# Kernel optimization log

Measured on AMD Instinct MI355X. Metric: run time of the kernel, lower is better.

Reference implementation:

```python
import jax, jax.numpy as jnp
import numpy as np

P_DROP = 0.31881923790897965  # torch.dropout p from the original module


def setup_inputs() -> dict:
    key = jax.random.key(0)
    k1, k2, k3, k4 = jax.random.split(key, 4)
    B, H, S, KV, D = 1, 16, 2048, 4096, 64  # KV = 2*S so the [S,2S] triu|tril mask lines up
    query = jax.random.normal(k1, (B, H, S, D), dtype=jnp.float32)
    key_t = jax.random.normal(k2, (B, H, KV, D), dtype=jnp.float32)
    value = jax.random.normal(k3, (B, H, KV, D), dtype=jnp.float32)
    # deterministic dropout keep-mask, keep prob = 1 - p
    drop_mask = jax.random.bernoulli(k4, 1.0 - P_DROP, (B, H, S, KV))
    return {"query": query, "key": key_t, "value": value, "drop_mask": drop_mask}


def _structured_mask(S, dtype):
    # torch.cat([triu(ones(S,S,bool),1), tril(ones(S,S,bool))], dim=-1) -> [S, 2S]
    # bool mask is ADDED to scores (promotes to 0/1 floats), exactly as in the original.
    triu = jnp.triu(jnp.ones((S, S), dtype=bool), 1)
    tril = jnp.tril(jnp.ones((S, S), dtype=bool))
    return jnp.concatenate([triu, tril], axis=-1).astype(dtype)  # [S, 2S]


def reference(query, key, value, drop_mask):
    B, H, S, D = query.shape
    scale = jnp.asarray(1.0 / np.sqrt(D), query.dtype)
    mask = _structured_mask(S, query.dtype)  # [S, 2S] of 0/1
    # qk: [B,H,S,KV]
    qk = jnp.einsum('bhsd,bhkd->bhsk', query, key) * scale + mask
    attn = jax.nn.softmax(qk, axis=-1)
    keep_scale = jnp.asarray(1.0 / (1.0 - P_DROP), attn.dtype)
    attn = jnp.where(drop_mask, attn * keep_scale, jnp.zeros((), attn.dtype))
    return jnp.einsum('bhsk,bhkd->bhsd', attn, value)
```

## Files before the change

kernel.cpp:

```cpp
#include <hip/hip_runtime.h>
#include <hip/hip_bf16.h>


#define H_   16
#define S_   2048
#define KV_  4096
#define D_   64
#define NSPLIT 2
#define CPB  32

using bf16x8 = __attribute__((ext_vector_type(8))) __bf16;
using bf16x4 = __attribute__((ext_vector_type(4))) __bf16;
using f32x4  = __attribute__((ext_vector_type(4))) float;
using uintx4 = __attribute__((ext_vector_type(4))) unsigned;

constexpr float KEEP_SCALE = (float)(1.0 / (1.0 - 0.31881923790897965));
#define C_SC  0.18033688011112043f
#define C_ONE -10.098865286222744f
#define C_ZRO -11.541560327111707f

#define WS_FLAG 0
#define WS_K    256
#define WS_V    (WS_K + 8388608)
#define WS_PART (WS_V + 8388608)
#define WS_LS   (WS_PART + 16777216)

__device__ __forceinline__ void gld16(const void* g, void* l) {
    __builtin_amdgcn_global_load_lds(
        (const __attribute__((address_space(1))) unsigned*)g,
        (__attribute__((address_space(3))) unsigned*)l, 16, 0, 0);
}

__global__ void detect_mask(const unsigned* __restrict__ m, int* __restrict__ flag) {
    __shared__ int bad;
    if (threadIdx.x == 0) bad = 0;
    __syncthreads();
    int ok = 1;
    for (int i = threadIdx.x; i < 4096; i += blockDim.x) {
        unsigned w = m[i];
        if (w > 1u && w != 0x3F800000u) ok = 0;
    }
    if (!ok) atomicOr(&bad, 1);
    __syncthreads();
    if (threadIdx.x == 0) *flag = bad;
}

__global__ __launch_bounds__(256)
void conv_k(const float* __restrict__ K, char* __restrict__ out) {
    const unsigned u = blockIdx.x * 256 + threadIdx.x;
    const unsigned w = u & 511;
    const unsigned row = w >> 3;
    const unsigned dcol = (((w & 7) * 16) ^ ((row & 7) << 4)) >> 1;
    const unsigned tile = u >> 9, h = tile >> 6, c = tile & 63;
    const float* src = K + (((size_t)h * KV_) + c * 64 + row) * D_ + dcol;
    f32x4 f0 = *(const f32x4*)src;
    f32x4 f1 = *(const f32x4*)(src + 4);
    bf16x8 b;
    #pragma unroll
    for (int e = 0; e < 4; ++e) { b[e] = (__bf16)f0[e]; b[4 + e] = (__bf16)f1[e]; }
    *(bf16x8*)(out + (size_t)u * 16) = b;
}

__global__ __launch_bounds__(256)
void conv_v(const float* __restrict__ V, char* __restrict__ out) {
    __shared__ __bf16 T[64][72];
    const int tile = blockIdx.x;
    const int h = tile >> 6, c = tile & 63;
    const float* src = V + ((size_t)h * KV_ + c * 64) * D_;
    const int tid = threadIdx.x;
    #pragma unroll
    for (int r = 0; r < 4; ++r) {
        const int off = r * 1024 + tid * 4;
        const int kv = off >> 6, d = off & 63;
        f32x4 f = *(const f32x4*)(src + off);
        #pragma unroll
        for (int e = 0; e < 4; ++e) T[d + e][kv] = (__bf16)f[e];
    }
    __syncthreads();
    char* dst = out + (size_t)tile * 8192;
    #pragma unroll
    for (int r = 0; r < 2; ++r) {
        const int u = r * 256 + tid;
        const int d = u >> 3;
        const int kv0 = ((((u & 7) * 16) ^ ((d & 7) << 4))) >> 1;
        *(bf16x8*)(dst + (size_t)u * 16) = *(const bf16x8*)&T[d][kv0];
    }
}

__global__ __launch_bounds__(512, 4)
void attn_fwd(const float* __restrict__ Q,
              const unsigned char* __restrict__ Mb,
              const int* __restrict__ flagp,
              const char* __restrict__ Ktiles,
              const char* __restrict__ Vtiles,
              float* __restrict__ Part,
              float* __restrict__ Ls)
{
    __shared__ char smem[49152];

    const int tid  = threadIdx.x;
    const int wave = tid >> 6, lane = tid & 63;
    const int lq   = lane & 15, g = lane >> 4;
    const int swz  = (lq & 7) << 4;

    const int b  = blockIdx.x;
    const int wg = (b & 7) * 64 + (b >> 3);
    const int h  = wg >> 5;
    const int qt = (wg >> 1) & 15, split = wg & 1;
    const int q0w = qt * 128 + wave * 16;
    const int q_g = q0w + lq;

    const bool byteMode = (*flagp != 0);
    const unsigned* Mw = (const unsigned*)Mb;

    bf16x8 bq[2];
    {
        const float* qrow = Q + ((size_t)h * S_ + q_g) * D_ + g * 8;
        #pragma unroll
        for (int kk = 0; kk < 2; ++kk) {
            f32x4 f0 = *(const f32x4*)(qrow + 32 * kk);
            f32x4 f1 = *(const f32x4*)(qrow + 32 * kk + 4);
            bf16x8 bb;
            #pragma unroll
            for (int e = 0; e < 4; ++e) { bb[e] = (__bf16)f0[e]; bb[4 + e] = (__bf16)f1[e]; }
            bq[kk] = bb;
        }
    }

    const char* gK = Ktiles + (size_t)h * 64 * 8192;
    const char* gV = Vtiles + (size_t)h * 64 * 8192;
    char* Pb = smem + 32768 + wave * 2048;

    float lsum = 0.f;
    f32x4 acc[4] = {};

    auto stage = [&](int buf, int c) {
        const char* sk = gK + (size_t)c * 8192 + tid * 16;
        const char* sv = gV + (size_t)c * 8192 + tid * 16;
        char* dk = smem + buf * 16384 + tid * 16;
        gld16(sk, dk);
        gld16(sv, dk + 8192);
    };

    unsigned mreg[16];
    auto load_bits = [&](int cc) {
        if (byteMode) {
            const unsigned char* base = Mb + ((size_t)h * S_ + q0w) * KV_ + (size_t)cc * 64 + lane;
            #pragma unroll
            for (int i = 0; i < 16; ++i) mreg[i] = base[(size_t)i * KV_];
        } else {
            const unsigned* base = Mw + ((size_t)h * S_ + q0w) * KV_ + (size_t)cc * 64 + lane;
            #pragma unroll
            for (int i = 0; i < 16; ++i) mreg[i] = base[(size_t)i * KV_];
        }
    };
    auto ballot_bits = [&]() -> unsigned long long {
        unsigned long long sav = 0;
        #pragma unroll
        for (int i = 0; i < 16; ++i) {
            unsigned long long bal = __ballot(mreg[i] != 0u);
            if (lq == i) sav = bal;
        }
        return sav;
    };

    const int cs = split * CPB, ce = cs + CPB;
    load_bits(cs);
    stage(0, cs);
    unsigned long long mb_cur = ballot_bits();
    __syncthreads();
    int cur = 0;

    for (int c = cs; c < ce; ++c) {
        const bool more = (c + 1 < ce);
        if (more) load_bits(c + 1);
        if (more) stage(cur ^ 1, c + 1);
        const unsigned long long mb = mb_cur;
        const char* Kb = smem + cur * 16384;
        const char* Vb = Kb + 8192;

        f32x4 st[4] = {};
        __builtin_amdgcn_s_setprio(1);
        #pragma unroll
        for (int t = 0; t < 4; ++t) {
            #pragma unroll
            for (int kk = 0; kk < 2; ++kk) {
                bf16x8 ak = *(const bf16x8*)(Kb + (16 * t + lq) * 128 + ((16 * g + 64 * kk) ^ swz));
                st[t] = __builtin_amdgcn_mfma_f32_16x16x32_bf16(ak, bq[kk], st[t], 0, 0, 0);
            }
        }
        __builtin_amdgcn_s_setprio(0);

        #pragma unroll
        for (int t = 0; t < 4; ++t) {
            bf16x4 pb;
            #pragma unroll
            for (int i = 0; i < 4; ++i) {
                const int kvl = 16 * t + 4 * g + i;
                const int kvg = c * 64 + kvl;
                const bool one = (kvg < S_) ? (kvg > q_g) : (kvg - S_ <= q_g);
                float v = fmaf(st[t][i], C_SC, one ? C_ONE : C_ZRO);
                float pp = exp2f(v);
                lsum += pp;
                pb[i] = (__bf16)(((mb >> kvl) & 1) ? pp : 0.f);
            }
            *(bf16x4*)(Pb + lq * 128 + ((32 * t + 8 * g) ^ swz)) = pb;
        }

        asm volatile("s_waitcnt lgkmcnt(0)" ::: "memory");
        __builtin_amdgcn_sched_barrier(0);

        __builtin_amdgcn_s_setprio(1);
        #pragma unroll
        for (int c2 = 0; c2 < 2; ++c2) {
            bf16x8 ap = *(const bf16x8*)(Pb + lq * 128 + ((64 * c2 + 16 * g) ^ swz));
            #pragma unroll
            for (int nt = 0; nt < 4; ++nt) {
                bf16x8 bv = *(const bf16x8*)(Vb + (16 * nt + lq) * 128 + ((64 * c2 + 16 * g) ^ swz));
                acc[nt] = __builtin_amdgcn_mfma_f32_16x16x32_bf16(ap, bv, acc[nt], 0, 0, 0);
            }
        }
        __builtin_amdgcn_s_setprio(0);

        if (more) mb_cur = ballot_bits();

        __syncthreads();
        cur ^= 1;
    }

    lsum += __shfl_xor(lsum, 16);
    lsum += __shfl_xor(lsum, 32);
    if (g == 0) Ls[((size_t)split * H_ + h) * S_ + q_g] = lsum;

    float* pa = Part + (((size_t)split * H_ + h) * S_ + q0w + 4 * g) * D_;
    #pragma unroll
    for (int i = 0; i < 4; ++i)
        #pragma unroll
        for (int nt = 0; nt < 4; ++nt)
            pa[i * D_ + nt * 16 + lq] = acc[nt][i];
}

__global__ __launch_bounds__(256)
void combine(const float* __restrict__ Part, const float* __restrict__ Ls,
             float* __restrict__ Out) {
    const int idx = blockIdx.x * 256 + threadIdx.x;
    const int r  = idx >> 4;
    const int dg = (idx & 15) * 4;
    const f32x4 a = *(const f32x4*)(Part + (size_t)r * D_ + dg);
    const f32x4 b = *(const f32x4*)(Part + (size_t)(H_ * S_ + r) * D_ + dg);
    const float l = Ls[r] + Ls[H_ * S_ + r];
    const float s = KEEP_SCALE / l;
    f32x4 o;
    #pragma unroll
    for (int e = 0; e < 4; ++e) o[e] = (a[e] + b[e]) * s;
    *(f32x4*)(Out + (size_t)r * D_ + dg) = o;
}

extern "C" void kernel_launch(void* const* d_in, const int* in_sizes, int n_in,
                              void* d_out, int out_size, void* d_ws, size_t ws_size,
                              hipStream_t stream) {
    const float* Q = (const float*)d_in[0];
    const float* K = (const float*)d_in[1];
    const float* V = (const float*)d_in[2];
    const unsigned char* M = (const unsigned char*)d_in[3];
    char* ws = (char*)d_ws;
    int* flag = (int*)(ws + WS_FLAG);
    char* kt = ws + WS_K;
    char* vt = ws + WS_V;
    float* part = (float*)(ws + WS_PART);
    float* ls = (float*)(ws + WS_LS);

    detect_mask<<<1, 256, 0, stream>>>((const unsigned*)M, flag);
    conv_k<<<2048, 256, 0, stream>>>(K, kt);
    conv_v<<<1024, 256, 0, stream>>>(V, vt);
    attn_fwd<<<512, 512, 0, stream>>>(Q, M, flag, kt, vt, part, ls);
    combine<<<2048, 256, 0, stream>>>(part, ls, (float*)d_out);
}
```

Baseline: 175.3 us.

## Halve workgroup size and batch dropout-mask loads four chunks at a time

The attention kernel now runs 1024 workgroups of 256 threads, each covering 64 query rows instead of 128, with the K/V staging done as four 16-byte copies per thread and LDS cut to 40 KB. The dropout mask is fetched as wide vector non-temporal loads covering four 64-column chunks at once, then ballot-packed into four bitmasks, replacing a narrow per-chunk load-and-ballot each iteration. The aim is more coalesced, higher-throughput reads of the large mask stream and better occupancy and scheduling from smaller blocks. In exchange it holds more registers for the mask data and launches twice as many blocks that each restage the same K/V tiles.

```diff
diff --git a/kernel.cpp b/kernel.cpp
--- a/kernel.cpp
+++ b/kernel.cpp
@@ -87,8 +87,7 @@
     }
 }
 
-__global__ __launch_bounds__(512, 4)
-void attn_fwd(const float* __restrict__ Q,
+__global__ void attn_fwd(const float* __restrict__ Q,
               const unsigned char* __restrict__ Mb,
               const int* __restrict__ flagp,
               const char* __restrict__ Ktiles,
@@ -96,7 +95,7 @@
               float* __restrict__ Part,
               float* __restrict__ Ls)
 {
-    __shared__ char smem[49152];
+    __shared__ char smem[40960];
 
     const int tid  = threadIdx.x;
     const int wave = tid >> 6, lane = tid & 63;
@@ -104,10 +103,10 @@
     const int swz  = (lq & 7) << 4;
 
     const int b  = blockIdx.x;
-    const int wg = (b & 7) * 64 + (b >> 3);
-    const int h  = wg >> 5;
-    const int qt = (wg >> 1) & 15, split = wg & 1;
-    const int q0w = qt * 128 + wave * 16;
+    const int wg = (b & 7) * 128 + (b >> 3);
+    const int h  = wg >> 6;
+    const int qt = (wg >> 1) & 31, split = wg & 1;
+    const int q0w = qt * 64 + wave * 16;
     const int q_g = q0w + lq;
 
     const bool byteMode = (*flagp != 0);
@@ -138,94 +137,108 @@
         const char* sk = gK + (size_t)c * 8192 + tid * 16;
         const char* sv = gV + (size_t)c * 8192 + tid * 16;
         char* dk = smem + buf * 16384 + tid * 16;
-        gld16(sk, dk);
-        gld16(sv, dk + 8192);
+        gld16(sk,        dk);
+        gld16(sk + 4096, dk + 4096);
+        gld16(sv,        dk + 8192);
+        gld16(sv + 4096, dk + 12288);
     };
 
-    unsigned mreg[16];
-    auto load_bits = [&](int cc) {
+    uintx4  mr[16];
+    unsigned mrb[16];
+    auto load_quad = [&](int c0) {
         if (byteMode) {
-            const unsigned char* base = Mb + ((size_t)h * S_ + q0w) * KV_ + (size_t)cc * 64 + lane;
-            #pragma unroll
-            for (int i = 0; i < 16; ++i) mreg[i] = base[(size_t)i * KV_];
+            const unsigned char* bp = Mb + ((size_t)h * S_ + q0w) * KV_ + (size_t)c0 * 64 + 4 * lane;
+            #pragma unroll
+            for (int r = 0; r < 16; ++r)
+                mrb[r] = __builtin_nontemporal_load((const unsigned*)(bp + (size_t)r * KV_));
         } else {
-            const unsigned* base = Mw + ((size_t)h * S_ + q0w) * KV_ + (size_t)cc * 64 + lane;
-            #pragma unroll
-            for (int i = 0; i < 16; ++i) mreg[i] = base[(size_t)i * KV_];
+            const unsigned* wp = Mw + ((size_t)h * S_ + q0w) * KV_ + (size_t)c0 * 64 + 4 * lane;
+            #pragma unroll
+            for (int r = 0; r < 16; ++r)
+                mr[r] = __builtin_nontemporal_load((const uintx4*)(wp + (size_t)r * KV_));
         }
     };
-    auto ballot_bits = [&]() -> unsigned long long {
-        unsigned long long sav = 0;
-        #pragma unroll
-        for (int i = 0; i < 16; ++i) {
-            unsigned long long bal = __ballot(mreg[i] != 0u);
-            if (lq == i) sav = bal;
-        }
-        return sav;
+    unsigned long long balv[4];
+    auto ballot_quad = [&]() {
+        #pragma unroll
+        for (int r = 0; r < 16; ++r) {
+            #pragma unroll
+            for (int j = 0; j < 4; ++j) {
+                const bool pred = byteMode ? (((mrb[r] >> (8 * j)) & 0xFFu) != 0u)
+                                           : (mr[r][j] != 0u);
+                unsigned long long bal = __ballot(pred);
+                if (lq == r) balv[j] = bal;
+            }
+        }
     };
 
     const int cs = split * CPB, ce = cs + CPB;
-    load_bits(cs);
+    load_quad(cs);
     stage(0, cs);
-    unsigned long long mb_cur = ballot_bits();
+    ballot_quad();
     __syncthreads();
     int cur = 0;
 
-    for (int c = cs; c < ce; ++c) {
-        const bool more = (c + 1 < ce);
-        if (more) load_bits(c + 1);
-        if (more) stage(cur ^ 1, c + 1);
-        const unsigned long long mb = mb_cur;
-        const char* Kb = smem + cur * 16384;
-        const char* Vb = Kb + 8192;
-
-        f32x4 st[4] = {};
-        __builtin_amdgcn_s_setprio(1);
-        #pragma unroll
-        for (int t = 0; t < 4; ++t) {
-            #pragma unroll
-            for (int kk = 0; kk < 2; ++kk) {
-                bf16x8 ak = *(const bf16x8*)(Kb + (16 * t + lq) * 128 + ((16 * g + 64 * kk) ^ swz));
-                st[t] = __builtin_amdgcn_mfma_f32_16x16x32_bf16(ak, bq[kk], st[t], 0, 0, 0);
-            }
-        }
-        __builtin_amdgcn_s_setprio(0);
-
-        #pragma unroll
-        for (int t = 0; t < 4; ++t) {
-            bf16x4 pb;
-            #pragma unroll
-            for (int i = 0; i < 4; ++i) {
-                const int kvl = 16 * t + 4 * g + i;
-                const int kvg = c * 64 + kvl;
-                const bool one = (kvg < S_) ? (kvg > q_g) : (kvg - S_ <= q_g);
-                float v = fmaf(st[t][i], C_SC, one ? C_ONE : C_ZRO);
-                float pp = exp2f(v);
-                lsum += pp;
-                pb[i] = (__bf16)(((mb >> kvl) & 1) ? pp : 0.f);
-            }
-            *(bf16x4*)(Pb + lq * 128 + ((32 * t + 8 * g) ^ swz)) = pb;
-        }
-
-        asm volatile("s_waitcnt lgkmcnt(0)" ::: "memory");
-        __builtin_amdgcn_sched_barrier(0);
-
-        __builtin_amdgcn_s_setprio(1);
-        #pragma unroll
-        for (int c2 = 0; c2 < 2; ++c2) {
-            bf16x8 ap = *(const bf16x8*)(Pb + lq * 128 + ((64 * c2 + 16 * g) ^ swz));
-            #pragma unroll
-            for (int nt = 0; nt < 4; ++nt) {
-                bf16x8 bv = *(const bf16x8*)(Vb + (16 * nt + lq) * 128 + ((64 * c2 + 16 * g) ^ swz));
-                acc[nt] = __builtin_amdgcn_mfma_f32_16x16x32_bf16(ap, bv, acc[nt], 0, 0, 0);
-            }
-        }
-        __builtin_amdgcn_s_setprio(0);
-
-        if (more) mb_cur = ballot_bits();
-
-        __syncthreads();
-        cur ^= 1;
+    for (int qd = 0; qd < CPB / 4; ++qd) {
+        const bool moreq = (qd + 1 < CPB / 4);
+        if (moreq) load_quad(cs + 4 * (qd + 1));
+
+        #pragma unroll
+        for (int g4 = 0; g4 < 4; ++g4) {
+            const int c = cs + 4 * qd + g4;
+            if (c + 1 < ce) stage(cur ^ 1, c + 1);
+            const char* Kb = smem + cur * 16384;
+            const char* Vb = Kb + 8192;
+
+            f32x4 st[4] = {};
+            __builtin_amdgcn_s_setprio(1);
+            #pragma unroll
+            for (int t = 0; t < 4; ++t) {
+                #pragma unroll
+                for (int kk = 0; kk < 2; ++kk) {
+                    bf16x8 ak = *(const bf16x8*)(Kb + (16 * t + lq) * 128 + ((16 * g + 64 * kk) ^ swz));
+                    st[t] = __builtin_amdgcn_mfma_f32_16x16x32_bf16(ak, bq[kk], st[t], 0, 0, 0);
+                }
+            }
+            __builtin_amdgcn_s_setprio(0);
+
+            const int shb = 16 * g4 + g;
+            #pragma unroll
+            for (int t = 0; t < 4; ++t) {
+                bf16x4 pb;
+                #pragma unroll
+                for (int i = 0; i < 4; ++i) {
+                    const int kvl = 16 * t + 4 * g + i;
+                    const int kvg = c * 64 + kvl;
+                    const bool one = (kvg < S_) ? (kvg > q_g) : (kvg - S_ <= q_g);
+                    float v = fmaf(st[t][i], C_SC, one ? C_ONE : C_ZRO);
+                    float pp = exp2f(v);
+                    lsum += pp;
+                    pb[i] = (__bf16)(((balv[i] >> (shb + 4 * t)) & 1) ? pp : 0.f);
+                }
+                *(bf16x4*)(Pb + lq * 128 + ((32 * t + 8 * g) ^ swz)) = pb;
+            }
+
+            asm volatile("s_waitcnt lgkmcnt(0)" ::: "memory");
+            __builtin_amdgcn_sched_barrier(0);
+
+            __builtin_amdgcn_s_setprio(1);
+            #pragma unroll
+            for (int c2 = 0; c2 < 2; ++c2) {
+                bf16x8 ap = *(const bf16x8*)(Pb + lq * 128 + ((64 * c2 + 16 * g) ^ swz));
+                #pragma unroll
+                for (int nt = 0; nt < 4; ++nt) {
+                    bf16x8 bv = *(const bf16x8*)(Vb + (16 * nt + lq) * 128 + ((64 * c2 + 16 * g) ^ swz));
+                    acc[nt] = __builtin_amdgcn_mfma_f32_16x16x32_bf16(ap, bv, acc[nt], 0, 0, 0);
+                }
+            }
+            __builtin_amdgcn_s_setprio(0);
+
+            __syncthreads();
+            cur ^= 1;
+        }
+
+        if (moreq) ballot_quad();
     }
 
     lsum += __shfl_xor(lsum, 16);
@@ -273,6 +286,6 @@
     detect_mask<<<1, 256, 0, stream>>>((const unsigned*)M, flag);
     conv_k<<<2048, 256, 0, stream>>>(K, kt);
     conv_v<<<1024, 256, 0, stream>>>(V, vt);
-    attn_fwd<<<512, 512, 0, stream>>>(Q, M, flag, kt, vt, part, ls);
+    attn_fwd<<<1024, 256, 0, stream>>>(Q, M, flag, kt, vt, part, ls);
     combine<<<2048, 256, 0, stream>>>(part, ls, (float*)d_out);
 }
```

Result: slower. 453.3 us (+158.5%).

## Triple-buffer K/V tiles and prefetch mask two chunks ahead with manual vmcnt waits

Applied to the files above, without the earlier changes.

Moves the K/V LDS staging from double to triple buffering and issues tile loads two chunks ahead. Dropout mask bits are likewise prefetched two chunks ahead, and __syncthreads is replaced with explicit s_waitcnt vmcnt counts plus s_barrier, so global loads stay in flight across iterations. The aim is to hide global-memory latency for the mask and tile loads. In exchange LDS grows from 48KB to 64KB, which may cut occupancy at 4 blocks per CU. The hand-counted vmcnt values are fragile: a wrong count can race or stall.

```diff
diff --git a/kernel.cpp b/kernel.cpp
--- a/kernel.cpp
+++ b/kernel.cpp
@@ -12,7 +12,6 @@
 using bf16x8 = __attribute__((ext_vector_type(8))) __bf16;
 using bf16x4 = __attribute__((ext_vector_type(4))) __bf16;
 using f32x4  = __attribute__((ext_vector_type(4))) float;
-using uintx4 = __attribute__((ext_vector_type(4))) unsigned;
 
 constexpr float KEEP_SCALE = (float)(1.0 / (1.0 - 0.31881923790897965));
 #define C_SC  0.18033688011112043f
@@ -96,7 +95,7 @@
               float* __restrict__ Part,
               float* __restrict__ Ls)
 {
-    __shared__ char smem[49152];
+    __shared__ char smem[65536];
 
     const int tid  = threadIdx.x;
     const int wave = tid >> 6, lane = tid & 63;
@@ -129,12 +128,13 @@
 
     const char* gK = Ktiles + (size_t)h * 64 * 8192;
     const char* gV = Vtiles + (size_t)h * 64 * 8192;
-    char* Pb = smem + 32768 + wave * 2048;
+    char* Pb = smem + 49152 + wave * 2048;
 
     float lsum = 0.f;
     f32x4 acc[4] = {};
 
-    auto stage = [&](int buf, int c) {
+    auto stage = [&](int c) {
+        const int buf = c % 3;
         const char* sk = gK + (size_t)c * 8192 + tid * 16;
         const char* sv = gV + (size_t)c * 8192 + tid * 16;
         char* dk = smem + buf * 16384 + tid * 16;
@@ -154,30 +154,36 @@
             for (int i = 0; i < 16; ++i) mreg[i] = base[(size_t)i * KV_];
         }
     };
-    auto ballot_bits = [&]() -> unsigned long long {
+    unsigned long long balv;
+    auto ballot_bits = [&]() {
         unsigned long long sav = 0;
         #pragma unroll
         for (int i = 0; i < 16; ++i) {
             unsigned long long bal = __ballot(mreg[i] != 0u);
             if (lq == i) sav = bal;
         }
-        return sav;
+        balv = sav;
     };
 
     const int cs = split * CPB, ce = cs + CPB;
+
     load_bits(cs);
-    stage(0, cs);
-    unsigned long long mb_cur = ballot_bits();
-    __syncthreads();
-    int cur = 0;
+    stage(cs);
+    stage(cs + 1);
+    asm volatile("s_waitcnt vmcnt(4)" ::: "memory");
+    __builtin_amdgcn_sched_barrier(0);
+    ballot_bits();
+    load_bits(cs + 1);
+    asm volatile("s_waitcnt vmcnt(18)" ::: "memory");
+    __builtin_amdgcn_sched_barrier(0);
+    __builtin_amdgcn_s_barrier();
 
     for (int c = cs; c < ce; ++c) {
-        const bool more = (c + 1 < ce);
-        if (more) load_bits(c + 1);
-        if (more) stage(cur ^ 1, c + 1);
-        const unsigned long long mb = mb_cur;
-        const char* Kb = smem + cur * 16384;
+        const bool m1 = (c + 1 < ce), m2 = (c + 2 < ce);
+        if (m2) stage(c + 2);
+        const char* Kb = smem + (c % 3) * 16384;
         const char* Vb = Kb + 8192;
+        const unsigned long long mb = balv;
 
         f32x4 st[4] = {};
         __builtin_amdgcn_s_setprio(1);
@@ -222,10 +228,20 @@
         }
         __builtin_amdgcn_s_setprio(0);
 
-        if (more) mb_cur = ballot_bits();
-
-        __syncthreads();
-        cur ^= 1;
+        if (m1) {
+            if (m2) { asm volatile("s_waitcnt vmcnt(2)" ::: "memory"); }
+            else    { asm volatile("s_waitcnt vmcnt(0)" ::: "memory"); }
+            __builtin_amdgcn_sched_barrier(0);
+            ballot_bits();
+            if (m2) load_bits(c + 2);
+        }
+
+        if (m1) {
+            if (m2) { asm volatile("s_waitcnt vmcnt(18)" ::: "memory"); }
+            else    { asm volatile("s_waitcnt vmcnt(0)" ::: "memory"); }
+            __builtin_amdgcn_sched_barrier(0);
+            __builtin_amdgcn_s_barrier();
+        }
     }
 
     lsum += __shfl_xor(lsum, 16);
```

Result: no change. 174.1 us (-0.7%).

## Double-buffer dropout mask registers and replace syncthreads with explicit vmcnt waits

Applied to the files above, without the earlier changes.

Unrolls the KV-chunk loop by two, using two register banks for the dropout-mask loads so the mask for chunk c+2 is in flight while chunk c is computed. Full __syncthreads is replaced by hand-placed s_waitcnt vmcnt counts plus s_barrier, so only the needed outstanding loads are waited on. The aim is to keep more global loads in flight and avoid the full-drain wait that syncthreads implies. The cost is more register use and fragile hard-coded vmcnt counts that must match the exact number of issued loads.

```diff
diff --git a/kernel.cpp b/kernel.cpp
--- a/kernel.cpp
+++ b/kernel.cpp
@@ -12,7 +12,6 @@
 using bf16x8 = __attribute__((ext_vector_type(8))) __bf16;
 using bf16x4 = __attribute__((ext_vector_type(4))) __bf16;
 using f32x4  = __attribute__((ext_vector_type(4))) float;
-using uintx4 = __attribute__((ext_vector_type(4))) unsigned;
 
 constexpr float KEEP_SCALE = (float)(1.0 / (1.0 - 0.31881923790897965));
 #define C_SC  0.18033688011112043f
@@ -142,41 +141,35 @@
         gld16(sv, dk + 8192);
     };
 
-    unsigned mreg[16];
-    auto load_bits = [&](int cc) {
-        if (byteMode) {
-            const unsigned char* base = Mb + ((size_t)h * S_ + q0w) * KV_ + (size_t)cc * 64 + lane;
-            #pragma unroll
-            for (int i = 0; i < 16; ++i) mreg[i] = base[(size_t)i * KV_];
-        } else {
-            const unsigned* base = Mw + ((size_t)h * S_ + q0w) * KV_ + (size_t)cc * 64 + lane;
-            #pragma unroll
-            for (int i = 0; i < 16; ++i) mreg[i] = base[(size_t)i * KV_];
-        }
-    };
-    auto ballot_bits = [&]() -> unsigned long long {
-        unsigned long long sav = 0;
-        #pragma unroll
-        for (int i = 0; i < 16; ++i) {
-            unsigned long long bal = __ballot(mreg[i] != 0u);
-            if (lq == i) sav = bal;
-        }
-        return sav;
-    };
-
-    const int cs = split * CPB, ce = cs + CPB;
-    load_bits(cs);
-    stage(0, cs);
-    unsigned long long mb_cur = ballot_bits();
-    __syncthreads();
-    int cur = 0;
-
-    for (int c = cs; c < ce; ++c) {
-        const bool more = (c + 1 < ce);
-        if (more) load_bits(c + 1);
-        if (more) stage(cur ^ 1, c + 1);
-        const unsigned long long mb = mb_cur;
-        const char* Kb = smem + cur * 16384;
+    unsigned mreg0[16], mreg1[16];
+    unsigned long long balv;
+
+    #define LOAD_BITS(MR, CC) do {                                                   \
+        if (byteMode) {                                                              \
+            const unsigned char* base_ = Mb + ((size_t)h * S_ + q0w) * KV_           \
+                                            + (size_t)(CC) * 64 + lane;              \
+            _Pragma("unroll")                                                        \
+            for (int i_ = 0; i_ < 16; ++i_) MR[i_] = base_[(size_t)i_ * KV_];        \
+        } else {                                                                     \
+            const unsigned* base_ = Mw + ((size_t)h * S_ + q0w) * KV_                \
+                                       + (size_t)(CC) * 64 + lane;                   \
+            _Pragma("unroll")                                                        \
+            for (int i_ = 0; i_ < 16; ++i_) MR[i_] = base_[(size_t)i_ * KV_];        \
+        }                                                                            \
+    } while (0)
+
+    #define BALLOT_BITS(MR) do {                                                     \
+        unsigned long long sav_ = 0;                                                 \
+        _Pragma("unroll")                                                            \
+        for (int i_ = 0; i_ < 16; ++i_) {                                            \
+            unsigned long long bal_ = __ballot(MR[i_] != 0u);                        \
+            if (lq == i_) sav_ = bal_;                                               \
+        }                                                                            \
+        balv = sav_;                                                                 \
+    } while (0)
+
+    auto body = [&](int c, int buf) {
+        const char* Kb = smem + buf * 16384;
         const char* Vb = Kb + 8192;
 
         f32x4 st[4] = {};
@@ -202,7 +195,7 @@
                 float v = fmaf(st[t][i], C_SC, one ? C_ONE : C_ZRO);
                 float pp = exp2f(v);
                 lsum += pp;
-                pb[i] = (__bf16)(((mb >> kvl) & 1) ? pp : 0.f);
+                pb[i] = (__bf16)(((balv >> kvl) & 1) ? pp : 0.f);
             }
             *(bf16x4*)(Pb + lq * 128 + ((32 * t + 8 * g) ^ swz)) = pb;
         }
@@ -221,12 +214,55 @@
             }
         }
         __builtin_amdgcn_s_setprio(0);
-
-        if (more) mb_cur = ballot_bits();
-
-        __syncthreads();
-        cur ^= 1;
-    }
+    };
+
+    const int cs = split * CPB;
+
+    LOAD_BITS(mreg0, cs);
+    stage(0, cs);
+    asm volatile("s_waitcnt vmcnt(2)" ::: "memory");
+    __builtin_amdgcn_sched_barrier(0);
+    BALLOT_BITS(mreg0);
+    LOAD_BITS(mreg1, cs + 1);
+    asm volatile("s_waitcnt vmcnt(16)" ::: "memory");
+    __builtin_amdgcn_sched_barrier(0);
+    __builtin_amdgcn_s_barrier();
+
+    for (int p = 0; p < CPB / 2; ++p) {
+        const int a = cs + 2 * p;
+        const bool lastp = (p + 1 >= CPB / 2);
+
+        stage(1, a + 1);
+        if (!lastp) LOAD_BITS(mreg0, a + 2);
+        __builtin_amdgcn_sched_barrier(0);
+        body(a, 0);
+        if (!lastp) { asm volatile("s_waitcnt vmcnt(18)" ::: "memory"); }
+        else        { asm volatile("s_waitcnt vmcnt(2)"  ::: "memory"); }
+        __builtin_amdgcn_sched_barrier(0);
+        BALLOT_BITS(mreg1);
+        if (!lastp) { asm volatile("s_waitcnt vmcnt(16)" ::: "memory"); }
+        else        { asm volatile("s_waitcnt vmcnt(0)"  ::: "memory"); }
+        __builtin_amdgcn_sched_barrier(0);
+        __builtin_amdgcn_s_barrier();
+
+        if (!lastp) {
+            stage(0, a + 2);
+            LOAD_BITS(mreg1, a + 3);
+        }
+        __builtin_amdgcn_sched_barrier(0);
+        body(a + 1, 1);
+        if (!lastp) {
+            asm volatile("s_waitcnt vmcnt(18)" ::: "memory");
+            __builtin_amdgcn_sched_barrier(0);
+            BALLOT_BITS(mreg0);
+            asm volatile("s_waitcnt vmcnt(16)" ::: "memory");
+            __builtin_amdgcn_sched_barrier(0);
+            __builtin_amdgcn_s_barrier();
+        }
+    }
+
+    #undef LOAD_BITS
+    #undef BALLOT_BITS
 
     lsum += __shfl_xor(lsum, 16);
     lsum += __shfl_xor(lsum, 32);
```

After: 318.6 us. +81.7%, slower.
